# Performance work log

Hardware: AMD Instinct MI355X
Metric: run time of the kernel (lower is better)

The kernel has to match this reference:

```python
import jax, jax.numpy as jnp
import numpy as np

D_MODEL = 1024
N_HEADS = 16
HEAD_DIM = D_MODEL // N_HEADS
INNER = 4 * D_MODEL  # mlp_ratio=4
EPS = 1e-5


def setup_inputs() -> dict:
    key = jax.random.key(0)
    ks = jax.random.split(key, 8)
    B, L = 2, 2048
    s = 0.02
    return {
        "x": jax.random.normal(ks[0], (B, L, D_MODEL), dtype=jnp.float32),
        "w_qkv": jax.random.normal(ks[1], (D_MODEL, 3 * D_MODEL), dtype=jnp.float32) * s,
        "b_qkv": jnp.zeros((3 * D_MODEL,), jnp.float32),
        "w_out": jax.random.normal(ks[2], (D_MODEL, D_MODEL), dtype=jnp.float32) * s,
        "b_out": jnp.zeros((D_MODEL,), jnp.float32),
        "w_fc1": jax.random.normal(ks[3], (D_MODEL, INNER), dtype=jnp.float32) * s,
        "b_fc1": jnp.zeros((INNER,), jnp.float32),
        "w_fc2": jax.random.normal(ks[4], (INNER, D_MODEL), dtype=jnp.float32) * s,
        "b_fc2": jnp.zeros((D_MODEL,), jnp.float32),
        "ln1_g": jnp.ones((D_MODEL,), jnp.float32),
        "ln1_b": jnp.zeros((D_MODEL,), jnp.float32),
        "ln2_g": jnp.ones((D_MODEL,), jnp.float32),
        "ln2_b": jnp.zeros((D_MODEL,), jnp.float32),
    }


def _layernorm(x, g, b):
    mu = jnp.mean(x, axis=-1, keepdims=True)
    var = jnp.mean(jnp.square(x - mu), axis=-1, keepdims=True)
    return (x - mu) * jax.lax.rsqrt(var + EPS) * g + b


def reference(x, w_qkv, b_qkv, w_out, b_out, w_fc1, b_fc1, w_fc2, b_fc2,
              ln1_g, ln1_b, ln2_g, ln2_b):
    B, L, D = x.shape
    scale = HEAD_DIM ** -0.5

    # --- attention (prefill, kv_cache=None, S=L) ---
    h = _layernorm(x, ln1_g, ln1_b)
    qkv = (h @ w_qkv + b_qkv).reshape(B, L, 3, N_HEADS, HEAD_DIM)
    q, k, v = (qkv[:, :, i].transpose(0, 2, 1, 3) for i in range(3))  # (B,H,L,hd)
    attn = jnp.einsum('bhqd,bhkd->bhqk', q, k) * scale
    causal = jnp.arange(L)[None, :] > jnp.arange(L)[:, None]  # col > row
    attn = jnp.where(causal[None, None], -jnp.inf, attn)
    attn = jax.nn.softmax(attn, axis=-1)
    o = jnp.einsum('bhqk,bhkd->bhqd', attn, v).transpose(0, 2, 1, 3).reshape(B, L, D)
    x = x + o @ w_out + b_out

    # --- MLP ---
    h2 = _layernorm(x, ln2_g, ln2_b)
    h2 = jax.nn.gelu(h2 @ w_fc1 + b_fc1, approximate=False)  # torch nn.GELU = exact erf
    x = x + h2 @ w_fc2 + b_fc2
    return x
```

## Files before the change

kernel.cpp:

```cpp
#include <hip/hip_runtime.h>
#include <hip/hip_bf16.h>

typedef unsigned short u16;
typedef unsigned int u32;
typedef short bf16x8 __attribute__((ext_vector_type(8)));
typedef float f32x4 __attribute__((ext_vector_type(4)));

#define SEQ 2048
#define DM 1024
#define NH 16
#define HD 64
#define INNER 4096
#define MTOT 4096
#define QKV_ELEMS 4194304

static __device__ __forceinline__ u16 f2bf(float f) {
  u32 u = __float_as_uint(f);
  u = (u + 0x7fffu + ((u >> 16) & 1u)) >> 16;
  return (u16)u;
}

static __device__ __forceinline__ void async_copy16(void* lds, const void* g) {
  __builtin_amdgcn_global_load_lds(
      (const __attribute__((address_space(1))) u32*)g,
      (__attribute__((address_space(3))) u32*)lds, 16, 0, 0);
}

#define MFMA16(a, b, c) __builtin_amdgcn_mfma_f32_16x16x32_bf16(a, b, c, 0, 0, 0)

__global__ __launch_bounds__(256) void transpose_cast(
    const float* __restrict__ src, u16* __restrict__ dst, int K, int N) {
  __shared__ float tile[32][33];
  int bx = blockIdx.x;
  int by = blockIdx.y;
  int t = threadIdx.x;
  int tr = t >> 5, tc = t & 31;
#pragma unroll
  for (int i = 0; i < 4; ++i) {
    int r = by * 32 + tr + i * 8;
    int c = bx * 32 + tc;
    tile[tr + i * 8][tc] = src[(size_t)r * N + c];
  }
  __syncthreads();
#pragma unroll
  for (int i = 0; i < 4; ++i) {
    int n = bx * 32 + tr + i * 8;
    int kk = by * 32 + tc;
    dst[(size_t)n * K + kk] = f2bf(tile[tc][tr + i * 8]);
  }
}

__global__ __launch_bounds__(256) void ln_kernel(
    const float* __restrict__ x, const float* __restrict__ g,
    const float* __restrict__ b, u16* __restrict__ out) {
  int row = blockIdx.x, t = threadIdx.x;
  const float* xr = x + (size_t)row * DM;
  float4 v = *(const float4*)(xr + t * 4);
  float s = v.x + v.y + v.z + v.w;
  float ss = v.x * v.x + v.y * v.y + v.z * v.z + v.w * v.w;
#pragma unroll
  for (int d = 1; d < 64; d <<= 1) {
    s += __shfl_xor(s, d);
    ss += __shfl_xor(ss, d);
  }
  __shared__ float red[8];
  int w = t >> 6, lane = t & 63;
  if (lane == 0) { red[w] = s; red[4 + w] = ss; }
  __syncthreads();
  s = red[0] + red[1] + red[2] + red[3];
  ss = red[4] + red[5] + red[6] + red[7];
  float mu = s * (1.f / DM);
  float var = ss * (1.f / DM) - mu * mu;
  float rstd = rsqrtf(var + 1e-5f);
  float4 gv = *(const float4*)(g + t * 4);
  float4 bv = *(const float4*)(b + t * 4);
  u32 p0 = (u32)f2bf((v.x - mu) * rstd * gv.x + bv.x) |
           ((u32)f2bf((v.y - mu) * rstd * gv.y + bv.y) << 16);
  u32 p1 = (u32)f2bf((v.z - mu) * rstd * gv.z + bv.z) |
           ((u32)f2bf((v.w - mu) * rstd * gv.w + bv.w) << 16);
  uint2 pk; pk.x = p0; pk.y = p1;
  *(uint2*)(out + (size_t)row * DM + t * 4) = pk;
}

template <int EPI, int BN>
__global__ __launch_bounds__(256) void gemm_bt(
    const u16* __restrict__ A, const u16* __restrict__ Bt,
    const float* __restrict__ bias, const float* __restrict__ resid,
    void* __restrict__ outp, int M, int N, int K) {
  constexpr int NF = BN / 32;
  __shared__ u16 As[2][128 * 32];
  __shared__ u16 Bs[2][BN * 32];
  int t = threadIdx.x;
  int lane = t & 63, w = t >> 6;
  int lo = lane & 15, hi = lane >> 4;
  int wr = w >> 1, wc = w & 1;
  int m0 = blockIdx.y * 128, n0 = blockIdx.x * BN;

  f32x4 acc[4][NF];
#pragma unroll
  for (int i = 0; i < 4; ++i)
#pragma unroll
    for (int j = 0; j < NF; ++j) acc[i][j] = f32x4{0.f, 0.f, 0.f, 0.f};

  const u16* gA = A + (size_t)(m0 + (t >> 2)) * K + (t & 3) * 8;
  const u16* gB = Bt + (size_t)(n0 + (t >> 2)) * K + (t & 3) * 8;

  auto STAGE = [&](int buf, int kt) {
    char* lA = (char*)(&As[buf][0]) + w * 1024;
    char* lB = (char*)(&Bs[buf][0]) + w * 1024;
    async_copy16(lA, gA + kt * 32);
    async_copy16(lA + 4096, gA + (size_t)64 * K + kt * 32);
    async_copy16(lB, gB + kt * 32);
    if constexpr (BN == 128)
      async_copy16(lB + 4096, gB + (size_t)64 * K + kt * 32);
  };

  int nk = K >> 5;
  int buf = 0;
  STAGE(0, 0);
  __syncthreads();

  for (int kt = 0; kt < nk; ++kt) {
    if (kt + 1 < nk) STAGE(buf ^ 1, kt + 1);
    bf16x8 af[4], bq[NF];
#pragma unroll
    for (int f = 0; f < 4; ++f)
      af[f] = *(const bf16x8*)(&As[buf][(wr * 64 + f * 16 + lo) * 32 + hi * 8]);
#pragma unroll
    for (int j = 0; j < NF; ++j)
      bq[j] = *(const bf16x8*)(&Bs[buf][(wc * (BN / 2) + j * 16 + lo) * 32 + hi * 8]);
#pragma unroll
    for (int i = 0; i < 4; ++i)
#pragma unroll
      for (int j = 0; j < NF; ++j)
        acc[i][j] = MFMA16(af[i], bq[j], acc[i][j]);
    __syncthreads();
    buf ^= 1;
  }

#pragma unroll
  for (int i = 0; i < 4; ++i) {
#pragma unroll
    for (int j = 0; j < NF; ++j) {
      int col = n0 + wc * (BN / 2) + j * 16 + lo;
#pragma unroll
      for (int r = 0; r < 4; ++r) {
        int m = m0 + wr * 64 + i * 16 + hi * 4 + r;
        float val = acc[i][j][r];
        if constexpr (EPI == 0) {
          val += bias[col];
          int which = col >> 10;
          int h = (col >> 6) & 15, d = col & 63;
          int b = m >> 11, l = m & 2047;
          size_t bh = (size_t)(b * NH + h);
          u16* qp = (u16*)outp;
          if (which == 0)
            qp[(bh * SEQ + l) * HD + d] = f2bf(val * 0.18033688011112043f);
          else if (which == 1)
            (qp + QKV_ELEMS)[(bh * SEQ + l) * HD + d] = f2bf(val);
          else
            (qp + 2 * QKV_ELEMS)[(bh * HD + d) * SEQ + l] = f2bf(val);
        } else if constexpr (EPI == 1) {
          val += bias[col] + resid[(size_t)m * N + col];
          ((float*)outp)[(size_t)m * N + col] = val;
        } else {
          val += bias[col];
          val = 0.5f * val * (1.0f + erff(val * 0.7071067811865476f));
          ((u16*)outp)[(size_t)m * N + col] = f2bf(val);
        }
      }
    }
  }
}

__global__ __launch_bounds__(256) void attn_kernel(
    const u16* __restrict__ q, const u16* __restrict__ k,
    const u16* __restrict__ vt, u16* __restrict__ o) {
  int bx = blockIdx.x, bh = blockIdx.y;
  int t = threadIdx.x;
  int lane = t & 63, w = t >> 6;
  int lo = lane & 15, hi = lane >> 4;

  __shared__ u16 Ks[2][4096];
  __shared__ u16 Vs[2][4096];
  __shared__ u16 Ps[4][1024];

  const char* kg = (const char*)(k + (size_t)bh * SEQ * HD);
  const char* vg = (const char*)(vt + (size_t)bh * HD * SEQ);
  int b = bh >> 4, h = bh & 15;

  u32 sw = (u32)((lo & 7) << 4);

  int koff[2], voff[2];
#pragma unroll
  for (int p = 0; p < 2; ++p) {
    int g = p * 256 + w * 64 + lane;
    int r = g >> 3, c = g & 7;
    int cs = c ^ (r & 7);
    koff[p] = r * 128 + cs * 16;
    voff[p] = r * 4096 + cs * 16;
  }

  bf16x8 ones;
#pragma unroll
  for (int i = 0; i < 8; ++i) ones[i] = (short)0x3F80;

#pragma unroll 1
  for (int pass = 0; pass < 2; ++pass) {
    int qt = pass == 0 ? (31 - bx) : bx;

    int qrow = qt * 64 + w * 16 + lo;
    const u16* qbase = q + ((size_t)bh * SEQ + qrow) * HD;
    bf16x8 qf0 = *(const bf16x8*)(qbase + hi * 8);
    bf16x8 qf1 = *(const bf16x8*)(qbase + 32 + hi * 8);

    f32x4 o_acc[4];
#pragma unroll
    for (int df = 0; df < 4; ++df) o_acc[df] = f32x4{0.f, 0.f, 0.f, 0.f};
    f32x4 o_sum = f32x4{0.f, 0.f, 0.f, 0.f};
    float m_run[4] = {-INFINITY, -INFINITY, -INFINITY, -INFINITY};

    auto STAGE = [&](int bb, int kt) {
#pragma unroll
      for (int p = 0; p < 2; ++p) {
        async_copy16((char*)&Ks[bb][0] + p * 4096 + w * 1024,
                     kg + (size_t)kt * 8192 + koff[p]);
        async_copy16((char*)&Vs[bb][0] + p * 4096 + w * 1024,
                     vg + (size_t)kt * 128 + voff[p]);
      }
    };

    int buf = 0;
    STAGE(0, 0);
    __syncthreads();

    for (int kt = 0; kt <= qt; ++kt) {
      if (kt < qt) STAGE(buf ^ 1, kt + 1);

      f32x4 s[4];
#pragma unroll
      for (int cf = 0; cf < 4; ++cf) {
        s[cf] = f32x4{0.f, 0.f, 0.f, 0.f};
        u32 ro = (u32)((cf * 16 + lo) * 128);
        bf16x8 kf0 = *(const bf16x8*)((char*)&Ks[buf][0] + ((ro + hi * 16) ^ sw));
        bf16x8 kf1 =
            *(const bf16x8*)((char*)&Ks[buf][0] + ((ro + 64 + hi * 16) ^ sw));
        s[cf] = MFMA16(qf0, kf0, s[cf]);
        s[cf] = MFMA16(qf1, kf1, s[cf]);
      }

      if (kt == qt) {
#pragma unroll
        for (int cf = 0; cf < 4; ++cf)
#pragma unroll
          for (int r = 0; r < 4; ++r) {
            int kcol = kt * 64 + cf * 16 + lo;
            int qr = qt * 64 + w * 16 + hi * 4 + r;
            if (kcol > qr) s[cf][r] = -INFINITY;
          }
      }

      float pmax[4];
#pragma unroll
      for (int r = 0; r < 4; ++r) {
        float v = fmaxf(fmaxf(s[0][r], s[1][r]), fmaxf(s[2][r], s[3][r]));
        v = fmaxf(v, __shfl_xor(v, 1));
        v = fmaxf(v, __shfl_xor(v, 2));
        v = fmaxf(v, __shfl_xor(v, 4));
        v = fmaxf(v, __shfl_xor(v, 8));
        pmax[r] = v;
      }

      int small = (pmax[0] <= m_run[0] + 8.f) & (pmax[1] <= m_run[1] + 8.f) &
                  (pmax[2] <= m_run[2] + 8.f) & (pmax[3] <= m_run[3] + 8.f);
      if (!__all(small)) {
#pragma unroll
        for (int r = 0; r < 4; ++r) {
          float mnew = fmaxf(m_run[r], pmax[r]);
          float a = exp2f(m_run[r] - mnew);
          m_run[r] = mnew;
          o_sum[r] *= a;
#pragma unroll
          for (int df = 0; df < 4; ++df) o_acc[df][r] *= a;
        }
      }

#pragma unroll
      for (int r = 0; r < 4; ++r) {
        int prow = hi * 4 + r;
        u32 pbase = (u32)(prow * 128);
        u32 psw = (u32)((prow & 7) << 4);
#pragma unroll
        for (int cf = 0; cf < 4; ++cf) {
          float p = exp2f(s[cf][r] - m_run[r]);
          u32 boff = pbase + (((u32)((cf * 16 + lo) * 2)) ^ psw);
          *(u16*)((char*)&Ps[w][0] + boff) = (u16)(__float_as_uint(p) >> 16);
        }
      }

#pragma unroll
      for (int ks = 0; ks < 2; ++ks) {
        u32 rboff = (u32)(lo * 128 + (((u32)(ks * 64 + hi * 16)) ^ sw));
        bf16x8 pf = *(const bf16x8*)((char*)&Ps[w][0] + rboff);
#pragma unroll
        for (int df = 0; df < 4; ++df) {
          u32 ro = (u32)((df * 16 + lo) * 128);
          bf16x8 vf = *(const bf16x8*)((char*)&Vs[buf][0] +
                                       ((ro + ks * 64 + hi * 16) ^ sw));
          o_acc[df] = MFMA16(pf, vf, o_acc[df]);
        }
        o_sum = MFMA16(pf, ones, o_sum);
      }

      __syncthreads();
      buf ^= 1;
    }

#pragma unroll
    for (int df = 0; df < 4; ++df) {
#pragma unroll
      for (int r = 0; r < 4; ++r) {
        float val = o_acc[df][r] / o_sum[r];
        int orow = qt * 64 + w * 16 + hi * 4 + r;
        size_t oidx = ((size_t)b * SEQ + orow) * DM + h * HD + df * 16 + lo;
        o[oidx] = f2bf(val);
      }
    }
  }
}

extern "C" void kernel_launch(void* const* d_in, const int* in_sizes, int n_in,
                              void* d_out, int out_size, void* d_ws,
                              size_t ws_size, hipStream_t stream) {
  const float* x = (const float*)d_in[0];
  const float* w_qkv = (const float*)d_in[1];
  const float* b_qkv = (const float*)d_in[2];
  const float* w_out = (const float*)d_in[3];
  const float* b_out = (const float*)d_in[4];
  const float* w_fc1 = (const float*)d_in[5];
  const float* b_fc1 = (const float*)d_in[6];
  const float* w_fc2 = (const float*)d_in[7];
  const float* b_fc2 = (const float*)d_in[8];
  const float* ln1_g = (const float*)d_in[9];
  const float* ln1_b = (const float*)d_in[10];
  const float* ln2_g = (const float*)d_in[11];
  const float* ln2_b = (const float*)d_in[12];
  float* out = (float*)d_out;

  char* ws = (char*)d_ws;
  const size_t MB = 1u << 20;
  u16* hb = (u16*)(ws + 0);
  u16* wqkvT = (u16*)(ws + 8 * MB);
  u16* woutT = (u16*)(ws + 14 * MB);
  u16* wfc1T = (u16*)(ws + 16 * MB);
  u16* wfc2T = (u16*)(ws + 24 * MB);
  u16* qb = (u16*)(ws + 32 * MB);
  u16* attn_o = (u16*)(ws + 56 * MB);
  float* x1 = (float*)(ws + 64 * MB);
  u16* gbuf = (u16*)(ws + 32 * MB);

  dim3 blk(256);

  transpose_cast<<<dim3(3072 / 32, 1024 / 32), blk, 0, stream>>>(w_qkv, wqkvT, 1024, 3072);
  transpose_cast<<<dim3(1024 / 32, 1024 / 32), blk, 0, stream>>>(w_out, woutT, 1024, 1024);
  transpose_cast<<<dim3(4096 / 32, 1024 / 32), blk, 0, stream>>>(w_fc1, wfc1T, 1024, 4096);
  transpose_cast<<<dim3(1024 / 32, 4096 / 32), blk, 0, stream>>>(w_fc2, wfc2T, 4096, 1024);

  ln_kernel<<<MTOT, blk, 0, stream>>>(x, ln1_g, ln1_b, hb);

  gemm_bt<0, 128><<<dim3(3072 / 128, MTOT / 128), blk, 0, stream>>>(
      hb, wqkvT, b_qkv, nullptr, qb, MTOT, 3072, 1024);

  attn_kernel<<<dim3(16, 32), blk, 0, stream>>>(
      qb, qb + QKV_ELEMS, qb + 2 * QKV_ELEMS, attn_o);

  gemm_bt<1, 64><<<dim3(1024 / 64, MTOT / 128), blk, 0, stream>>>(
      attn_o, woutT, b_out, x, x1, MTOT, 1024, 1024);

  ln_kernel<<<MTOT, blk, 0, stream>>>(x1, ln2_g, ln2_b, hb);

  gemm_bt<2, 128><<<dim3(4096 / 128, MTOT / 128), blk, 0, stream>>>(
      hb, wfc1T, b_fc1, nullptr, gbuf, MTOT, 4096, 1024);

  gemm_bt<1, 64><<<dim3(1024 / 64, MTOT / 128), blk, 0, stream>>>(
      gbuf, wfc2T, b_fc2, x1, out, MTOT, 1024, 4096);
}
```

Measured before the change: 397.3 us.

## Triple-buffer GEMM LDS staging with partial vmcnt waits and XCD-aware block swizzle

Converts the bf16 GEMM main loop from double to triple buffering, issuing async global-to-LDS loads two k-tiles ahead. The full __syncthreads is replaced by an s_waitcnt on only the older tile's loads plus a raw barrier, so global latency overlaps more MFMA work. It also remaps workgroup IDs so consecutive blocks are spread across the 8 XCDs, which may change L2 reuse. In exchange it uses more LDS per block, which can reduce occupancy. The swizzle assumes the block count divides by 8, and the hand-coded vmcnt values must match the number of loads issued per stage.

```diff
diff --git a/kernel.cpp b/kernel.cpp
--- a/kernel.cpp
+++ b/kernel.cpp
@@ -88,13 +88,18 @@
     const float* __restrict__ bias, const float* __restrict__ resid,
     void* __restrict__ outp, int M, int N, int K) {
   constexpr int NF = BN / 32;
-  __shared__ u16 As[2][128 * 32];
-  __shared__ u16 Bs[2][BN * 32];
+  __shared__ u16 As[3][128 * 32];
+  __shared__ u16 Bs[3][BN * 32];
   int t = threadIdx.x;
   int lane = t & 63, w = t >> 6;
   int lo = lane & 15, hi = lane >> 4;
   int wr = w >> 1, wc = w & 1;
-  int m0 = blockIdx.y * 128, n0 = blockIdx.x * BN;
+
+  int lin = blockIdx.y * gridDim.x + blockIdx.x;
+  int nwg = gridDim.x * gridDim.y;
+  int qq = nwg >> 3;
+  int wg = (lin & 7) * qq + (lin >> 3);
+  int m0 = (wg / gridDim.x) * 128, n0 = (wg % gridDim.x) * BN;
 
   f32x4 acc[4][NF];
 #pragma unroll
@@ -114,28 +119,45 @@
     if constexpr (BN == 128)
       async_copy16(lB + 4096, gB + (size_t)64 * K + kt * 32);
   };
+  auto WAIT_LPS = [&]() {
+    if constexpr (BN == 128)
+      asm volatile("s_waitcnt vmcnt(4)" ::: "memory");
+    else
+      asm volatile("s_waitcnt vmcnt(3)" ::: "memory");
+  };
 
   int nk = K >> 5;
-  int buf = 0;
   STAGE(0, 0);
-  __syncthreads();
-
+  STAGE(1, 1);
+  WAIT_LPS();
+  __builtin_amdgcn_s_barrier();
+  __builtin_amdgcn_sched_barrier(0);
+
+  int cur = 0;
   for (int kt = 0; kt < nk; ++kt) {
-    if (kt + 1 < nk) STAGE(buf ^ 1, kt + 1);
+    if (kt + 2 < nk) STAGE((kt + 2) % 3, kt + 2);
     bf16x8 af[4], bq[NF];
 #pragma unroll
     for (int f = 0; f < 4; ++f)
-      af[f] = *(const bf16x8*)(&As[buf][(wr * 64 + f * 16 + lo) * 32 + hi * 8]);
+      af[f] = *(const bf16x8*)(&As[cur][(wr * 64 + f * 16 + lo) * 32 + hi * 8]);
 #pragma unroll
     for (int j = 0; j < NF; ++j)
-      bq[j] = *(const bf16x8*)(&Bs[buf][(wc * (BN / 2) + j * 16 + lo) * 32 + hi * 8]);
+      bq[j] =
+          *(const bf16x8*)(&Bs[cur][(wc * (BN / 2) + j * 16 + lo) * 32 + hi * 8]);
 #pragma unroll
     for (int i = 0; i < 4; ++i)
 #pragma unroll
       for (int j = 0; j < NF; ++j)
         acc[i][j] = MFMA16(af[i], bq[j], acc[i][j]);
-    __syncthreads();
-    buf ^= 1;
+    if (kt + 1 < nk) {
+      if (kt + 2 < nk)
+        WAIT_LPS();
+      else
+        asm volatile("s_waitcnt vmcnt(0)" ::: "memory");
+      __builtin_amdgcn_s_barrier();
+      __builtin_amdgcn_sched_barrier(0);
+    }
+    cur = (cur == 2) ? 0 : cur + 1;
   }
 
 #pragma unroll
```

Result: slower. 416.8 us (+4.9%).
